# Kernel tuning notes

Hardware: AMD Instinct MI355X
Metric: run time of the kernel (lower is better)

Reference implementation:

```python
import jax, jax.numpy as jnp
import numpy as np

N_NODES = 100000
N_EDGES = 600000
D_IN = 128
D_OUT = 128


def setup_inputs() -> dict:
    key = jax.random.key(0)
    k1, k2, k3, k4, k5, k6 = jax.random.split(key, 6)
    node_feature = jax.random.normal(k1, (N_NODES, D_IN), dtype=jnp.float32)
    edge_indices = jax.random.randint(k2, (2, N_EDGES), 0, N_NODES, dtype=jnp.int64)
    scale = 1.0 / np.sqrt(D_IN)
    W_line = jax.random.uniform(k3, (D_OUT, D_IN), jnp.float32, -scale, scale)
    b_line = jax.random.uniform(k4, (D_OUT,), jnp.float32, -scale, scale)
    W_self = jax.random.uniform(k5, (D_OUT, D_IN), jnp.float32, -scale, scale)
    b_self = jax.random.uniform(k6, (D_OUT,), jnp.float32, -scale, scale)
    return {
        "node_feature": node_feature,
        "edge_indices": edge_indices,
        "W_line": W_line,
        "b_line": b_line,
        "W_self": W_self,
        "b_self": b_self,
    }


def reference(node_feature, edge_indices, W_line, b_line, W_self, b_self):
    source = edge_indices[0]
    target = edge_indices[1]
    # gather source features along edges: [E, D_in]
    src_feat = node_feature[source]
    # scatter-mean into target nodes (torch_scatter mean: sum / max(count,1))
    seg_sum = jax.ops.segment_sum(src_feat, target, num_segments=N_NODES)
    count = jax.ops.segment_sum(
        jnp.ones((src_feat.shape[0],), dtype=node_feature.dtype),
        target, num_segments=N_NODES)
    mean = seg_sum / jnp.maximum(count, 1.0)[:, None]
    # neighbour linear + self linear
    out = (mean @ W_line.T + b_line) + (node_feature @ W_self.T + b_self)
    return out
```

## Files before the change

### kernel.cpp

```cpp
#include <hip/hip_runtime.h>

#define N_NODES 100000
#define N_EDGES 600000
#define D 128
#define M_PAD 100096

#define NB   196
#define BWID 512
#define NCH  196
#define CE   3062
#define SCAN_N (NB * NCH)
#define SCAN_BLK 151

typedef unsigned int uint32;
typedef unsigned long long uint64;
typedef __attribute__((ext_vector_type(8))) short short8;
typedef __attribute__((ext_vector_type(4))) float f32x4;

__device__ __forceinline__ uint32 f2bf(float x) {
    uint32 u = __float_as_uint(x);
    return (u + 0x7FFFu + ((u >> 16) & 1u)) >> 16;
}
__device__ __forceinline__ float bflo(uint32 u) { return __uint_as_float(u << 16); }
__device__ __forceinline__ float bfhi(uint32 u) { return __uint_as_float(u & 0xFFFF0000u); }

__global__ __launch_bounds__(256) void k1_convert_count(
        const float* __restrict__ nf, unsigned short* __restrict__ AbufN,
        const int* __restrict__ edges, uint32* __restrict__ cntmat,
        uint64* __restrict__ flags) {
    __shared__ uint32 c[NB];
    const int tid = threadIdx.x;
    const int bid = blockIdx.x;

    if (bid == 1023 && tid < SCAN_BLK) flags[tid] = 0ULL;

    for (int idx = bid * 256 + tid; idx < N_NODES * 16; idx += 1024 * 256) {
        int r = idx >> 4;
        int ccol = (idx & 15) * 8;
        const float4 v0 = *reinterpret_cast<const float4*>(nf + (size_t)r * D + ccol);
        const float4 v1 = *reinterpret_cast<const float4*>(nf + (size_t)r * D + ccol + 4);
        uint4 w;
        w.x = f2bf(v0.x) | (f2bf(v0.y) << 16);
        w.y = f2bf(v0.z) | (f2bf(v0.w) << 16);
        w.z = f2bf(v1.x) | (f2bf(v1.y) << 16);
        w.w = f2bf(v1.z) | (f2bf(v1.w) << 16);
        *reinterpret_cast<uint4*>(AbufN + (size_t)r * 128 + ccol) = w;
    }

    if (bid < NCH) {
        for (int i = tid; i < NB; i += 256) c[i] = 0u;
        __syncthreads();
        const int e0 = bid * CE;
        const int e1 = (e0 + CE < N_EDGES) ? e0 + CE : N_EDGES;
        for (int e = e0 + tid; e < e1; e += 256) {
            int tgt = edges[N_EDGES + e];
            atomicAdd(&c[tgt >> 9], 1u);
        }
        __syncthreads();
        for (int i = tid; i < NB; i += 256)
            cntmat[(size_t)i * NCH + bid] = c[i];
    }
}

__global__ __launch_bounds__(256) void k2_scan(
        uint32* __restrict__ cntmat, uint64* __restrict__ flags,
        const float* __restrict__ Wl, const float* __restrict__ Ws,
        const float* __restrict__ bl, const float* __restrict__ bs,
        unsigned short* __restrict__ WcF, float* __restrict__ biasc) {
    const int gidx = blockIdx.x * 256 + threadIdx.x;
    if (gidx < 4096) {
        int lane = gidx & 63, f2 = gidx >> 6;
        int ks = f2 & 7, nn = (f2 >> 3) & 3, ch = f2 >> 5;
        int j = ch * 64 + nn * 16 + (lane & 15);
        int kb = ks * 32 + (lane >> 4) * 8;
        const float* srcp = (kb < D) ? (Wl + (size_t)j * D + kb)
                                     : (Ws + (size_t)j * D + (kb - D));
        const float4 v0 = *reinterpret_cast<const float4*>(srcp);
        const float4 v1 = *reinterpret_cast<const float4*>(srcp + 4);
        uint4 w;
        w.x = f2bf(v0.x) | (f2bf(v0.y) << 16);
        w.y = f2bf(v0.z) | (f2bf(v0.w) << 16);
        w.z = f2bf(v1.x) | (f2bf(v1.y) << 16);
        w.w = f2bf(v1.z) | (f2bf(v1.w) << 16);
        *reinterpret_cast<uint4*>(WcF + (size_t)gidx * 8) = w;
    }
    if (gidx < D) biasc[gidx] = bl[gidx] + bs[gidx];

    __shared__ uint32 s[256];
    __shared__ uint32 r2[256];
    const int t = threadIdx.x;
    const int b = blockIdx.x;
    const int i = b * 256 + t;
    const uint32 v = (i < SCAN_N) ? cntmat[i] : 0u;
    s[t] = v;
    __syncthreads();
    for (int d = 1; d < 256; d <<= 1) {
        uint32 add = (t >= d) ? s[t - d] : 0u;
        __syncthreads();
        s[t] += add;
        __syncthreads();
    }
    const uint32 incl = s[t];
    const uint32 total = s[255];
    if (t == 0) atomicExch(&flags[b], (1ULL << 32) | (uint64)total);
    uint32 agg = 0;
    if (t < b) {
        uint64 fv;
        do { fv = atomicAdd(&flags[t], 0ULL); } while ((fv >> 32) == 0ULL);
        agg = (uint32)fv;
    }
    r2[t] = agg;
    __syncthreads();
    for (int d2 = 128; d2 > 0; d2 >>= 1) {
        if (t < d2) r2[t] += r2[t + d2];
        __syncthreads();
    }
    if (i < SCAN_N) cntmat[i] = r2[0] + incl - v;
}

__global__ __launch_bounds__(256) void k3_bucket(
        const int* __restrict__ edges, const uint32* __restrict__ base,
        uint32* __restrict__ bpair) {
    __shared__ uint32 c[NB];
    __shared__ uint32 bb[NB];
    const int t = threadIdx.x;
    const int cid = blockIdx.x;
    for (int i = t; i < NB; i += 256) {
        c[i] = 0u;
        bb[i] = base[(size_t)i * NCH + cid];
    }
    __syncthreads();
    const int e0 = cid * CE;
    const int e1 = (e0 + CE < N_EDGES) ? e0 + CE : N_EDGES;
    for (int e = e0 + t; e < e1; e += 256) {
        uint32 src = (uint32)edges[e];
        uint32 tgt = (uint32)edges[N_EDGES + e];
        uint32 bkt = tgt >> 9;
        uint32 r = atomicAdd(&c[bkt], 1u);
        uint32 pos = bb[bkt] + r;
        *reinterpret_cast<uint2*>(&bpair[2 * (size_t)pos]) = make_uint2(src, tgt);
    }
}

__global__ __launch_bounds__(256) void k4_csr(
        const uint32* __restrict__ bpair, const uint32* __restrict__ base,
        uint32* __restrict__ off, uint32* __restrict__ sorted_src) {
    __shared__ uint32 h[BWID];
    __shared__ uint32 h2[BWID];
    __shared__ uint32 pr[256];
    const int t = threadIdx.x;
    const int b = blockIdx.x;
    const uint32 start = base[(size_t)b * NCH];
    const uint32 end = (b == NB - 1) ? N_EDGES : base[(size_t)(b + 1) * NCH];
    for (int i = t; i < BWID; i += 256) { h[i] = 0u; h2[i] = 0u; }
    __syncthreads();
    for (uint32 e = start + t; e < end; e += 256) {
        uint32 tgt = bpair[2 * (size_t)e + 1];
        atomicAdd(&h[tgt & (BWID - 1)], 1u);
    }
    __syncthreads();
    const uint32 e0c = h[2 * t];
    const uint32 e1c = h[2 * t + 1];
    pr[t] = e0c + e1c;
    __syncthreads();
    for (int d = 1; d < 256; d <<= 1) {
        uint32 add = (t >= d) ? pr[t - d] : 0u;
        __syncthreads();
        pr[t] += add;
        __syncthreads();
    }
    const uint32 exb = (t > 0) ? pr[t - 1] : 0u;
    const int node0 = b * BWID + 2 * t;
    if (node0 < N_NODES) off[node0] = start + exb;
    if (node0 + 1 < N_NODES) off[node0 + 1] = start + exb + e0c;
    if (b == NB - 1 && t == 0) off[N_NODES] = N_EDGES;
    h[2 * t] = exb;
    h[2 * t + 1] = exb + e0c;
    __syncthreads();
    for (uint32 e = start + t; e < end; e += 256) {
        uint2 pq = *reinterpret_cast<const uint2*>(&bpair[2 * (size_t)e]);
        uint32 lt = pq.y & (BWID - 1);
        uint32 r = atomicAdd(&h2[lt], 1u);
        sorted_src[start + h[lt] + r] = pq.x;
    }
}

__global__ __launch_bounds__(512) void k_fused(
        const unsigned short* __restrict__ AbufN,
        const uint32* __restrict__ off,
        const uint32* __restrict__ sorted_src,
        const unsigned short* __restrict__ WcF,
        const float* __restrict__ biasc,
        float* __restrict__ out) {
    __shared__ unsigned short WcL[32768];
    __shared__ unsigned short Am[8192];
    const int tid = threadIdx.x;
    const int wave = tid >> 6;
    const int lane = tid & 63;
    const int row0 = blockIdx.x * 64;

#pragma unroll
    for (int i = 0; i < 8; ++i) {
        const int o = (i * 512 + tid) * 8;
        *reinterpret_cast<short8*>(&WcL[o]) = *reinterpret_cast<const short8*>(WcF + o);
    }

    const int sub = (lane >> 4) & 1;
    const int cl  = lane & 15;
    const int g   = lane >> 5;

#define LD(s) (*reinterpret_cast<const uint4*>(AbufN + (size_t)(s) * 128 + cl * 8))
#define ACC(a, u) { a[0] += bflo(u.x); a[1] += bfhi(u.x); a[2] += bflo(u.y); a[3] += bfhi(u.y); \
                    a[4] += bflo(u.z); a[5] += bfhi(u.z); a[6] += bflo(u.w); a[7] += bfhi(u.w); }

    for (int pr = 0; pr < 4; ++pr) {
        const int nl = wave * 8 + pr * 2 + g;
        const int node = row0 + nl;
        float aA[8] = {0.f,0.f,0.f,0.f,0.f,0.f,0.f,0.f};
        float aB[8] = {0.f,0.f,0.f,0.f,0.f,0.f,0.f,0.f};
        uint32 d = 0;
        if (node < N_NODES) {
            const uint32 o = off[node];
            d = off[node + 1] - o;
            const uint32* __restrict__ src = sorted_src + o;
            uint32 j = 0;
            for (; j + 8 <= d; j += 8) {
                uint32 s0 = src[j + 0 + sub];
                uint32 s1 = src[j + 2 + sub];
                uint32 s2 = src[j + 4 + sub];
                uint32 s3 = src[j + 6 + sub];
                uint4 u0 = LD(s0); uint4 u1 = LD(s1); uint4 u2 = LD(s2); uint4 u3 = LD(s3);
                ACC(aA, u0); ACC(aA, u1); ACC(aB, u2); ACC(aB, u3);
            }
            if (j < d) {
                const uint32 dm1 = d - 1;
                uint32 i0 = j + 0 + sub, i1 = j + 2 + sub, i2 = j + 4 + sub, i3 = j + 6 + sub;
                uint32 s0 = src[i0 < dm1 ? i0 : dm1];
                uint32 s1 = src[i1 < dm1 ? i1 : dm1];
                uint32 s2 = src[i2 < dm1 ? i2 : dm1];
                uint32 s3 = src[i3 < dm1 ? i3 : dm1];
                uint4 u0 = LD(s0); uint4 u1 = LD(s1); uint4 u2 = LD(s2); uint4 u3 = LD(s3);
                if (i0 >= d) { u0.x = 0u; u0.y = 0u; u0.z = 0u; u0.w = 0u; }
                if (i1 >= d) { u1.x = 0u; u1.y = 0u; u1.z = 0u; u1.w = 0u; }
                if (i2 >= d) { u2.x = 0u; u2.y = 0u; u2.z = 0u; u2.w = 0u; }
                if (i3 >= d) { u3.x = 0u; u3.y = 0u; u3.z = 0u; u3.w = 0u; }
                ACC(aA, u0); ACC(aA, u1); ACC(aB, u2); ACC(aB, u3);
            }
        }
#pragma unroll
        for (int r = 0; r < 8; ++r) {
            aA[r] += aB[r];
            aA[r] += __shfl_xor(aA[r], 16);
        }
        if (sub == 0) {
            const float inv = 1.0f / (float)(d > 0u ? d : 1u);
            uint4 w;
            w.x = f2bf(aA[0] * inv) | (f2bf(aA[1] * inv) << 16);
            w.y = f2bf(aA[2] * inv) | (f2bf(aA[3] * inv) << 16);
            w.z = f2bf(aA[4] * inv) | (f2bf(aA[5] * inv) << 16);
            w.w = f2bf(aA[6] * inv) | (f2bf(aA[7] * inv) << 16);
            *reinterpret_cast<uint4*>(&Am[nl * 128 + ((cl ^ (nl & 7)) * 8)]) = w;
        }
    }
#undef LD
#undef ACC
    __syncthreads();

    const int rg  = wave >> 1;
    const int chh = wave & 1;
    const int lr  = lane & 15;
    const int lkq = lane >> 4;
    const int lk  = lkq * 8;
    const int arow = rg * 16 + lr;

    f32x4 acc[4];
#pragma unroll
    for (int n = 0; n < 4; ++n) acc[n] = (f32x4){0.f, 0.f, 0.f, 0.f};

#pragma unroll
    for (int ks = 0; ks < 4; ++ks) {
        const int c0 = lkq + ks * 4;
        short8 a = *reinterpret_cast<const short8*>(
            &Am[arow * 128 + ((c0 ^ (arow & 7)) * 8)]);
#pragma unroll
        for (int n = 0; n < 4; ++n) {
            short8 b = *reinterpret_cast<const short8*>(
                &WcL[((chh * 32 + n * 8 + ks) * 64 + lane) * 8]);
            acc[n] = __builtin_amdgcn_mfma_f32_16x16x32_bf16(a, b, acc[n], 0, 0, 0);
        }
    }
    const unsigned short* pa = AbufN + (size_t)(row0 + arow) * 128 + lk;
#pragma unroll
    for (int ks = 4; ks < 8; ++ks) {
        short8 a = *reinterpret_cast<const short8*>(pa + (ks - 4) * 32);
#pragma unroll
        for (int n = 0; n < 4; ++n) {
            short8 b = *reinterpret_cast<const short8*>(
                &WcL[((chh * 32 + n * 8 + ks) * 64 + lane) * 8]);
            acc[n] = __builtin_amdgcn_mfma_f32_16x16x32_bf16(a, b, acc[n], 0, 0, 0);
        }
    }

    float bv[4];
#pragma unroll
    for (int n = 0; n < 4; ++n) bv[n] = biasc[chh * 64 + n * 16 + lr];

    const int rq = lkq * 4;
#pragma unroll
    for (int r = 0; r < 4; ++r) {
        const int row = row0 + rg * 16 + rq + r;
        if (row < N_NODES) {
            float* orow = out + (size_t)row * D + chh * 64;
#pragma unroll
            for (int n = 0; n < 4; ++n)
                orow[n * 16 + lr] = acc[n][r] + bv[n];
        }
    }
}

extern "C" void kernel_launch(void* const* d_in, const int* in_sizes, int n_in,
                              void* d_out, int out_size, void* d_ws, size_t ws_size,
                              hipStream_t stream) {
    const float* nf    = (const float*)d_in[0];
    const int*   edges = (const int*)d_in[1];
    const float* Wl    = (const float*)d_in[2];
    const float* bl    = (const float*)d_in[3];
    const float* Ws    = (const float*)d_in[4];
    const float* bs    = (const float*)d_in[5];
    float* out = (float*)d_out;

    char* p = (char*)d_ws;
    unsigned short* AbufN = (unsigned short*)p; p += (size_t)M_PAD * 128 * sizeof(unsigned short);
    uint32* cntmat     = (uint32*)p; p += (size_t)(SCAN_N + 64) * sizeof(uint32);
    uint32* bpair      = (uint32*)p; p += (size_t)2 * N_EDGES * sizeof(uint32);
    uint32* sorted_src = (uint32*)p; p += (size_t)N_EDGES * sizeof(uint32);
    uint32* off        = (uint32*)p; p += (size_t)(N_NODES + 8) * sizeof(uint32);
    uint64* flags      = (uint64*)p; p += 2048;
    unsigned short* WcF = (unsigned short*)p; p += (size_t)D * 256 * sizeof(unsigned short);
    float* biasc       = (float*)p;

    k1_convert_count<<<1024, 256, 0, stream>>>(nf, AbufN, edges, cntmat, flags);
    k2_scan<<<SCAN_BLK, 256, 0, stream>>>(cntmat, flags, Wl, Ws, bl, bs, WcF, biasc);
    k3_bucket<<<NCH, 256, 0, stream>>>(edges, cntmat, bpair);
    k4_csr<<<NB, 256, 0, stream>>>(bpair, cntmat, off, sorted_src);
    k_fused<<<(N_NODES + 63) / 64, 512, 0, stream>>>(AbufN, off, sorted_src, WcF, biasc, out);
}
```

Before: 95.64 us.

## Pack bucketed edge pairs into one word and prefetch first gather batch

The bucket pass now stores each edge as a single 32-bit word, holding the local target (9 bits) above a 17-bit source index, instead of an 8-byte pair. This halves the bpair traffic written by k3 and read twice by k4. The fused aggregation kernel also loads all four node offsets and the first eight source indices for every node pair up front, then issues the first feature gathers for two nodes at once, to expose more memory-level parallelism. This raises register pressure and relies on node indices fitting in 17 bits.

```diff
diff --git a/kernel.cpp b/kernel.cpp
--- a/kernel.cpp
+++ b/kernel.cpp
@@ -137,8 +137,7 @@
         uint32 tgt = (uint32)edges[N_EDGES + e];
         uint32 bkt = tgt >> 9;
         uint32 r = atomicAdd(&c[bkt], 1u);
-        uint32 pos = bb[bkt] + r;
-        *reinterpret_cast<uint2*>(&bpair[2 * (size_t)pos]) = make_uint2(src, tgt);
+        bpair[bb[bkt] + r] = ((tgt & 511u) << 17) | src;
     }
 }
 
@@ -155,8 +154,7 @@
     for (int i = t; i < BWID; i += 256) { h[i] = 0u; h2[i] = 0u; }
     __syncthreads();
     for (uint32 e = start + t; e < end; e += 256) {
-        uint32 tgt = bpair[2 * (size_t)e + 1];
-        atomicAdd(&h[tgt & (BWID - 1)], 1u);
+        atomicAdd(&h[bpair[e] >> 17], 1u);
     }
     __syncthreads();
     const uint32 e0c = h[2 * t];
@@ -178,10 +176,10 @@
     h[2 * t + 1] = exb + e0c;
     __syncthreads();
     for (uint32 e = start + t; e < end; e += 256) {
-        uint2 pq = *reinterpret_cast<const uint2*>(&bpair[2 * (size_t)e]);
-        uint32 lt = pq.y & (BWID - 1);
+        uint32 pq = bpair[e];
+        uint32 lt = pq >> 17;
         uint32 r = atomicAdd(&h2[lt], 1u);
-        sorted_src[start + h[lt] + r] = pq.x;
+        sorted_src[start + h[lt] + r] = pq & 0x1FFFFu;
     }
 }
 
@@ -213,53 +211,94 @@
 #define ACC(a, u) { a[0] += bflo(u.x); a[1] += bfhi(u.x); a[2] += bflo(u.y); a[3] += bfhi(u.y); \
                     a[4] += bflo(u.z); a[5] += bfhi(u.z); a[6] += bflo(u.w); a[7] += bfhi(u.w); }
 
-    for (int pr = 0; pr < 4; ++pr) {
-        const int nl = wave * 8 + pr * 2 + g;
+    uint32 oo[4], dd[4];
+#pragma unroll
+    for (int pr2 = 0; pr2 < 4; ++pr2) {
+        const int nl = wave * 8 + pr2 * 2 + g;
         const int node = row0 + nl;
-        float aA[8] = {0.f,0.f,0.f,0.f,0.f,0.f,0.f,0.f};
-        float aB[8] = {0.f,0.f,0.f,0.f,0.f,0.f,0.f,0.f};
-        uint32 d = 0;
-        if (node < N_NODES) {
-            const uint32 o = off[node];
-            d = off[node + 1] - o;
-            const uint32* __restrict__ src = sorted_src + o;
-            uint32 j = 0;
-            for (; j + 8 <= d; j += 8) {
-                uint32 s0 = src[j + 0 + sub];
-                uint32 s1 = src[j + 2 + sub];
-                uint32 s2 = src[j + 4 + sub];
-                uint32 s3 = src[j + 6 + sub];
-                uint4 u0 = LD(s0); uint4 u1 = LD(s1); uint4 u2 = LD(s2); uint4 u3 = LD(s3);
-                ACC(aA, u0); ACC(aA, u1); ACC(aB, u2); ACC(aB, u3);
+        const int nn = (node < N_NODES) ? node : (N_NODES - 1);
+        const uint32 o0 = off[nn];
+        const uint32 o1 = off[nn + 1];
+        oo[pr2] = o0;
+        dd[pr2] = (node < N_NODES) ? (o1 - o0) : 0u;
+    }
+    uint32 sx[4][4];
+#pragma unroll
+    for (int pr2 = 0; pr2 < 4; ++pr2) {
+        const uint32 d0 = dd[pr2];
+        const uint32 dm = d0 ? d0 - 1u : 0u;
+        const uint32* sp = sorted_src + oo[pr2];
+#pragma unroll
+        for (int k = 0; k < 4; ++k) {
+            uint32 i = 2u * (uint32)k + (uint32)sub;
+            sx[pr2][k] = sp[i < dm ? i : dm];
+        }
+    }
+#pragma unroll
+    for (int pr2 = 0; pr2 < 4; ++pr2)
+#pragma unroll
+        for (int k = 0; k < 4; ++k)
+            if (2u * (uint32)k + (uint32)sub >= dd[pr2]) sx[pr2][k] = 0u;
+
+#pragma unroll
+    for (int pg = 0; pg < 2; ++pg) {
+        uint4 u[2][4];
+#pragma unroll
+        for (int pp = 0; pp < 2; ++pp) {
+            const int pr2 = pg * 2 + pp;
+#pragma unroll
+            for (int k = 0; k < 4; ++k) u[pp][k] = LD(sx[pr2][k]);
+        }
+#pragma unroll
+        for (int pp = 0; pp < 2; ++pp) {
+            const int pr2 = pg * 2 + pp;
+            const uint32 d0 = dd[pr2];
+            float aA[8] = {0.f,0.f,0.f,0.f,0.f,0.f,0.f,0.f};
+            float aB[8] = {0.f,0.f,0.f,0.f,0.f,0.f,0.f,0.f};
+#pragma unroll
+            for (int k = 0; k < 4; ++k)
+                if (2u * (uint32)k + (uint32)sub >= d0) u[pp][k] = make_uint4(0u,0u,0u,0u);
+            ACC(aA, u[pp][0]); ACC(aB, u[pp][1]); ACC(aA, u[pp][2]); ACC(aB, u[pp][3]);
+
+            const uint32* sp = sorted_src + oo[pr2];
+            uint32 j = 8;
+            for (; j + 8 <= d0; j += 8) {
+                uint32 s0 = sp[j + 0 + sub];
+                uint32 s1 = sp[j + 2 + sub];
+                uint32 s2 = sp[j + 4 + sub];
+                uint32 s3 = sp[j + 6 + sub];
+                uint4 v0 = LD(s0); uint4 v1 = LD(s1); uint4 v2 = LD(s2); uint4 v3 = LD(s3);
+                ACC(aA, v0); ACC(aB, v1); ACC(aA, v2); ACC(aB, v3);
             }
-            if (j < d) {
-                const uint32 dm1 = d - 1;
+            if (j < d0) {
+                const uint32 dm1 = d0 - 1;
                 uint32 i0 = j + 0 + sub, i1 = j + 2 + sub, i2 = j + 4 + sub, i3 = j + 6 + sub;
-                uint32 s0 = src[i0 < dm1 ? i0 : dm1];
-                uint32 s1 = src[i1 < dm1 ? i1 : dm1];
-                uint32 s2 = src[i2 < dm1 ? i2 : dm1];
-                uint32 s3 = src[i3 < dm1 ? i3 : dm1];
-                uint4 u0 = LD(s0); uint4 u1 = LD(s1); uint4 u2 = LD(s2); uint4 u3 = LD(s3);
-                if (i0 >= d) { u0.x = 0u; u0.y = 0u; u0.z = 0u; u0.w = 0u; }
-                if (i1 >= d) { u1.x = 0u; u1.y = 0u; u1.z = 0u; u1.w = 0u; }
-                if (i2 >= d) { u2.x = 0u; u2.y = 0u; u2.z = 0u; u2.w = 0u; }
-                if (i3 >= d) { u3.x = 0u; u3.y = 0u; u3.z = 0u; u3.w = 0u; }
-                ACC(aA, u0); ACC(aA, u1); ACC(aB, u2); ACC(aB, u3);
+                uint32 s0 = sp[i0 < dm1 ? i0 : dm1];
+                uint32 s1 = sp[i1 < dm1 ? i1 : dm1];
+                uint32 s2 = sp[i2 < dm1 ? i2 : dm1];
+                uint32 s3 = sp[i3 < dm1 ? i3 : dm1];
+                uint4 v0 = LD(s0); uint4 v1 = LD(s1); uint4 v2 = LD(s2); uint4 v3 = LD(s3);
+                if (i0 >= d0) v0 = make_uint4(0u,0u,0u,0u);
+                if (i1 >= d0) v1 = make_uint4(0u,0u,0u,0u);
+                if (i2 >= d0) v2 = make_uint4(0u,0u,0u,0u);
+                if (i3 >= d0) v3 = make_uint4(0u,0u,0u,0u);
+                ACC(aA, v0); ACC(aB, v1); ACC(aA, v2); ACC(aB, v3);
             }
-        }
-#pragma unroll
-        for (int r = 0; r < 8; ++r) {
-            aA[r] += aB[r];
-            aA[r] += __shfl_xor(aA[r], 16);
-        }
-        if (sub == 0) {
-            const float inv = 1.0f / (float)(d > 0u ? d : 1u);
-            uint4 w;
-            w.x = f2bf(aA[0] * inv) | (f2bf(aA[1] * inv) << 16);
-            w.y = f2bf(aA[2] * inv) | (f2bf(aA[3] * inv) << 16);
-            w.z = f2bf(aA[4] * inv) | (f2bf(aA[5] * inv) << 16);
-            w.w = f2bf(aA[6] * inv) | (f2bf(aA[7] * inv) << 16);
-            *reinterpret_cast<uint4*>(&Am[nl * 128 + ((cl ^ (nl & 7)) * 8)]) = w;
+#pragma unroll
+            for (int r = 0; r < 8; ++r) {
+                aA[r] += aB[r];
+                aA[r] += __shfl_xor(aA[r], 16);
+            }
+            if (sub == 0) {
+                const int nl = wave * 8 + pr2 * 2 + g;
+                const float inv = 1.0f / (float)(dd[pr2] > 0u ? dd[pr2] : 1u);
+                uint4 w;
+                w.x = f2bf(aA[0] * inv) | (f2bf(aA[1] * inv) << 16);
+                w.y = f2bf(aA[2] * inv) | (f2bf(aA[3] * inv) << 16);
+                w.z = f2bf(aA[4] * inv) | (f2bf(aA[5] * inv) << 16);
+                w.w = f2bf(aA[6] * inv) | (f2bf(aA[7] * inv) << 16);
+                *reinterpret_cast<uint4*>(&Am[nl * 128 + ((cl ^ (nl & 7)) * 8)]) = w;
+            }
         }
     }
 #undef LD
@@ -332,7 +371,7 @@
     char* p = (char*)d_ws;
     unsigned short* AbufN = (unsigned short*)p; p += (size_t)M_PAD * 128 * sizeof(unsigned short);
     uint32* cntmat     = (uint32*)p; p += (size_t)(SCAN_N + 64) * sizeof(uint32);
-    uint32* bpair      = (uint32*)p; p += (size_t)2 * N_EDGES * sizeof(uint32);
+    uint32* bpair      = (uint32*)p; p += (size_t)N_EDGES * sizeof(uint32);
     uint32* sorted_src = (uint32*)p; p += (size_t)N_EDGES * sizeof(uint32);
     uint32* off        = (uint32*)p; p += (size_t)(N_NODES + 8) * sizeof(uint32);
     uint64* flags      = (uint64*)p; p += 2048;
```

Result: faster. 87.55 us (-8.5%).
